# Optimization experiments

Hardware: AMD Instinct MI355X
Metric: run time of the kernel (lower is better)

## Reference

```python
import jax, jax.numpy as jnp
import numpy as np

EPS = 1e-8


def setup_inputs() -> dict:
    key = jax.random.key(0)
    ks = jax.random.split(key, 4)
    B, Cin, Cout, K, S, H, W = 16, 256, 256, 3, 512, 128, 128
    return {
        "x": jax.random.normal(ks[0], (B, Cin, H, W), dtype=jnp.float32),
        "style": jax.random.normal(ks[1], (B, S), dtype=jnp.float32),
        "weight": jax.random.normal(ks[2], (1, Cout, Cin, K, K), dtype=jnp.float32),
        "mod_w": jax.random.normal(ks[3], (Cin, S), dtype=jnp.float32) * (1.0 / np.sqrt(S)),
        "mod_b": jnp.zeros((Cin,), dtype=jnp.float32),
        "bias": jnp.zeros((1, Cout, 1, 1), dtype=jnp.float32),
    }


def reference(x, style, weight, mod_w, mod_b, bias):
    B, Cin, H, W = x.shape
    _, Cout, _, K, _ = weight.shape
    scale = 1.0 / np.sqrt(Cin * K * K)

    # modulation: Linear(style_dim -> in_channel)
    s = style @ mod_w.T + mod_b                      # [B, Cin]
    w = scale * weight * s[:, None, :, None, None]   # [B, Cout, Cin, K, K]
    demod = jax.lax.rsqrt(jnp.sum(w * w, axis=(2, 3, 4)) + EPS)  # [B, Cout]
    w = w * demod[:, :, None, None, None]

    # grouped conv with groups = batch (per-sample weights)
    w = w.reshape(B * Cout, Cin, K, K)
    xg = x.reshape(1, B * Cin, H, W)
    out = jax.lax.conv_general_dilated(
        xg, w,
        window_strides=(1, 1),
        padding=[(1, 1), (1, 1)],
        dimension_numbers=("NCHW", "OIHW", "NCHW"),
        feature_group_count=B,
    )
    Ho, Wo = out.shape[2], out.shape[3]
    out = out.reshape(B, Cout, Ho, Wo)
    return out + bias
```

## Files before the change

kernel.cpp:

```cpp
#include <hip/hip_runtime.h>
#include <stdint.h>

typedef unsigned short u16;
typedef __attribute__((ext_vector_type(8))) short short8;
typedef __attribute__((ext_vector_type(4))) float f32x4;

#define AS1 __attribute__((address_space(1)))
#define AS3 __attribute__((address_space(3)))

static __device__ __forceinline__ void gload_lds16(const void* g, void* l) {
  __builtin_amdgcn_global_load_lds((const AS1 void*)g, (AS3 void*)l, 16, 0, 0);
}

static __device__ __forceinline__ u16 bf16r(float f) {
  union { float f; uint32_t u; } c; c.f = f;
  uint32_t u = c.u;
  u += 0x7fffu + ((u >> 16) & 1u);
  return (u16)(u >> 16);
}

static constexpr int NB = 16, CIN = 256, COUT = 256, HW = 128, SDIM = 512;
static constexpr float SCALE = 1.0f / 48.0f;

__global__ void k_style(const float* __restrict__ style, const float* __restrict__ mod_w,
                        const float* __restrict__ mod_b, float* __restrict__ s) {
  int b = blockIdx.x, ci = threadIdx.x;
  const float4* st = (const float4*)(style + (size_t)b * SDIM);
  const float4* mw = (const float4*)(mod_w + (size_t)ci * SDIM);
  float acc = 0.f;
  #pragma unroll 4
  for (int j = 0; j < SDIM / 4; ++j) {
    float4 a = st[j], w = mw[j];
    acc += a.x * w.x + a.y * w.y + a.z * w.z + a.w * w.w;
  }
  s[b * CIN + ci] = acc + mod_b[ci];
}

__global__ void k_wmod(const float* __restrict__ weight, const float* __restrict__ s,
                       u16* __restrict__ Wb) {
  __shared__ float wld[CIN * 9];
  __shared__ float red[8];
  int bid = blockIdx.x;
  int b = bid >> 8, co = bid & 255;
  int t = threadIdx.x;
  const float* wsrc = weight + (size_t)co * (CIN * 9);
  for (int i = t; i < CIN * 9; i += 256) wld[i] = wsrc[i];
  __syncthreads();
  int ci = t;
  float sv = s[b * CIN + ci];
  float v[9];
  float sq = 0.f;
  #pragma unroll
  for (int k = 0; k < 9; ++k) {
    float w = SCALE * wld[ci * 9 + k] * sv;
    v[k] = w;
    sq += w * w;
  }
  #pragma unroll
  for (int off = 32; off; off >>= 1) sq += __shfl_down(sq, off);
  int lane = t & 63, wid = t >> 6;
  if (lane == 0) red[wid] = sq;
  __syncthreads();
  if (t == 0) red[4] = rsqrtf(red[0] + red[1] + red[2] + red[3] + 1e-8f);
  __syncthreads();
  float demod = red[4];
  #pragma unroll
  for (int k = 0; k < 9; ++k) {
    Wb[(((size_t)b * 9 + k) * COUT + co) * CIN + ci] = bf16r(v[k] * demod);
  }
}

__global__ void k_xt(const float* __restrict__ x, u16* __restrict__ xTp) {
  __shared__ u16 T[128 * 65];
  int bid = blockIdx.x;
  int b = bid >> 7, h = bid & 127;
  int t = threadIdx.x;
  size_t rowbase = ((size_t)b * 130 + (h + 1)) * 130 * CIN;
  xTp[rowbase + t] = 0;
  xTp[rowbase + (size_t)129 * CIN + t] = 0;
  if (h == 0) {
    uint32_t* g = (uint32_t*)(xTp + (size_t)b * 130 * 130 * CIN);
    for (int i = t; i < 130 * CIN / 2; i += 256) g[i] = 0;
  }
  if (h == 127) {
    uint32_t* g = (uint32_t*)(xTp + ((size_t)b * 130 + 129) * 130 * CIN);
    for (int i = t; i < 130 * CIN / 2; i += 256) g[i] = 0;
  }
  for (int ci0 = 0; ci0 < CIN; ci0 += 64) {
    __syncthreads();
    #pragma unroll
    for (int i = 0; i < 8; ++i) {
      int idx = t + i * 256;
      int ci = idx >> 5, px4 = idx & 31;
      float4 v = *(const float4*)(x + (((size_t)b * CIN + ci0 + ci) * HW + h) * HW + px4 * 4);
      T[(px4 * 4 + 0) * 65 + ci] = bf16r(v.x);
      T[(px4 * 4 + 1) * 65 + ci] = bf16r(v.y);
      T[(px4 * 4 + 2) * 65 + ci] = bf16r(v.z);
      T[(px4 * 4 + 3) * 65 + ci] = bf16r(v.w);
    }
    __syncthreads();
    int ci = t & 63, pxo = t >> 6;
    #pragma unroll
    for (int i = 0; i < 32; ++i) {
      int px = i * 4 + pxo;
      xTp[rowbase + (size_t)(px + 1) * CIN + ci0 + ci] = T[px * 65 + ci];
    }
  }
}

static constexpr int SLOT = 12288;

__global__ __launch_bounds__(256, 2) void k_conv(const u16* __restrict__ Wb,
                                                 const u16* __restrict__ xTp,
                                                 const float* __restrict__ bias,
                                                 float* __restrict__ out) {
  extern __shared__ u16 lds[];
  int bid = blockIdx.x;
  int swz = (bid & 7) * 256 + (bid >> 3);
  int b = swz >> 7, r = swz & 127;
  int c2 = r >> 6, hp = r & 63;
  int h0 = hp * 2, co0 = c2 * 128;

  int t = threadIdx.x, lane = t & 63, wid = t >> 6;
  int wc = wid;
  int l15 = lane & 15;
  int row0 = wid * 16 + (lane >> 2);
  int sq8 = ((lane & 3) ^ ((lane >> 3) & 3)) << 3;
  int aswz = (((lane >> 4) ^ ((l15 >> 1) & 3))) << 3;
  const u16* Ab = Wb + (size_t)b * 9 * 65536;
  const u16* Bx = xTp + (size_t)b * 130 * 130 * 256;

  f32x4 acc[8][4];
  #pragma unroll
  for (int i = 0; i < 8; ++i)
    #pragma unroll
    for (int j = 0; j < 4; ++j) acc[i][j] = (f32x4)0.f;

#define STAGE(KT, SN)                                                            \
  do {                                                                           \
    int kpos_ = (KT) >> 3, ci0_ = ((KT) & 7) << 5;                               \
    int kh_ = kpos_ < 3 ? 0 : (kpos_ < 6 ? 1 : 2);                               \
    int kw_ = kpos_ - kh_ * 3;                                                   \
    const u16* As_ = Ab + (size_t)kpos_ * 65536 +                                \
                     (size_t)(co0 + row0) * 256 + ci0_ + sq8;                    \
    gload_lds16(As_,         (SN) + wid * 512 + lane * 8);                       \
    gload_lds16(As_ + 16384, (SN) + 2048 + wid * 512 + lane * 8);                \
    _Pragma("unroll")                                                            \
    for (int i_ = 0; i_ < 4; ++i_) {                                             \
      int r_ = i_ * 64 + row0;                                                   \
      const u16* Bs_ = Bx + ((size_t)(h0 + kh_ + (r_ >> 7)) * 130 + kw_          \
                             + (r_ & 127)) * 256 + ci0_ + sq8;                   \
      gload_lds16(Bs_, (SN) + 4096 + i_ * 2048 + wid * 512 + lane * 8);          \
    }                                                                            \
  } while (0)

#define KTBODY(KT, SCUR, SNXT)                                                   \
  {                                                                              \
    if ((KT) + 1 < 72) STAGE((KT) + 1, SNXT);                                    \
    short8 af_[8], bf_[4];                                                       \
    _Pragma("unroll")                                                            \
    for (int mt = 0; mt < 8; ++mt)                                               \
      af_[mt] = *(const short8*)&(SCUR)[mt * 512 + l15 * 32 + aswz];             \
    _Pragma("unroll")                                                            \
    for (int nt = 0; nt < 4; ++nt)                                               \
      bf_[nt] = *(const short8*)&(SCUR)[4096 + wc * 2048 + nt * 512              \
                                        + l15 * 32 + aswz];                      \
    __builtin_amdgcn_s_setprio(1);                                               \
    _Pragma("unroll")                                                            \
    for (int mt = 0; mt < 8; ++mt)                                               \
      _Pragma("unroll")                                                          \
      for (int nt = 0; nt < 4; ++nt)                                             \
        acc[mt][nt] = __builtin_amdgcn_mfma_f32_16x16x32_bf16(af_[mt], bf_[nt],  \
                                                              acc[mt][nt], 0, 0, 0); \
    __builtin_amdgcn_s_setprio(0);                                               \
    __syncthreads();                                                             \
  }

  u16* S0 = lds;
  u16* S1 = lds + SLOT;
  STAGE(0, S0);
  __syncthreads();

  #pragma unroll 1
  for (int kt = 0; kt < 72; kt += 2) {
    KTBODY(kt, S0, S1);
    KTBODY(kt + 1, S1, S0);
  }
#undef STAGE
#undef KTBODY

  #pragma unroll
  for (int mt = 0; mt < 8; ++mt) {
    #pragma unroll
    for (int j = 0; j < 4; ++j) {
      int co = co0 + mt * 16 + ((lane >> 4) * 4) + j;
      float bv = bias[co];
      #pragma unroll
      for (int nt = 0; nt < 4; ++nt) {
        int px = wc * 64 + nt * 16 + l15;
        int h = h0 + (px >> 7), w = px & 127;
        out[(((size_t)b * COUT + co) * HW + h) * HW + w] = acc[mt][nt][j] + bv;
      }
    }
  }
}

extern "C" void kernel_launch(void* const* d_in, const int* in_sizes, int n_in,
                              void* d_out, int out_size, void* d_ws, size_t ws_size,
                              hipStream_t stream) {
  const float* x      = (const float*)d_in[0];
  const float* style  = (const float*)d_in[1];
  const float* weight = (const float*)d_in[2];
  const float* mod_w  = (const float*)d_in[3];
  const float* mod_b  = (const float*)d_in[4];
  const float* bias   = (const float*)d_in[5];
  float* out = (float*)d_out;

  char* ws = (char*)d_ws;
  float* s   = (float*)ws;
  u16* Wb    = (u16*)(ws + 16384);
  u16* xTp   = (u16*)(ws + 16384 + (size_t)NB * 9 * COUT * CIN * 2);

  k_style<<<NB, 256, 0, stream>>>(style, mod_w, mod_b, s);
  k_wmod<<<NB * COUT, 256, 0, stream>>>(weight, s, Wb);
  k_xt<<<NB * HW, 256, 0, stream>>>(x, xTp);
  k_conv<<<NB * 2 * (HW / 2), 256, 2 * SLOT * 2, stream>>>(Wb, xTp, bias, out);
}
```

Baseline: 495.8 us.

## Retile conv to 256 channels by one row per block and vectorize xT stores

The conv kernel's block tile changes from 128 output channels by two image rows to all 256 output channels by a single row of 128 pixels. Waves are arranged 2x2 over channels and pixels, and the A/B staging in LDS is rearranged to match. Each input row slice is now loaded once for all channels, cutting redundant activation traffic, while the A/B tile ratio and total load per block shift. Separately, the transpose kernel now writes 16-byte vectors instead of scalar u16 stores.

```diff
diff --git a/kernel.cpp b/kernel.cpp
--- a/kernel.cpp
+++ b/kernel.cpp
@@ -86,6 +86,7 @@
     uint32_t* g = (uint32_t*)(xTp + ((size_t)b * 130 + 129) * 130 * CIN);
     for (int i = t; i < 130 * CIN / 2; i += 256) g[i] = 0;
   }
+  int c8 = t & 7, pxb = t >> 3;
   for (int ci0 = 0; ci0 < CIN; ci0 += 64) {
     __syncthreads();
     #pragma unroll
@@ -99,11 +100,13 @@
       T[(px4 * 4 + 3) * 65 + ci] = bf16r(v.w);
     }
     __syncthreads();
-    int ci = t & 63, pxo = t >> 6;
-    #pragma unroll
-    for (int i = 0; i < 32; ++i) {
-      int px = i * 4 + pxo;
-      xTp[rowbase + (size_t)(px + 1) * CIN + ci0 + ci] = T[px * 65 + ci];
+    #pragma unroll
+    for (int i = 0; i < 4; ++i) {
+      int px = i * 32 + pxb;
+      short8 v;
+      #pragma unroll
+      for (int j = 0; j < 8; ++j) v[j] = (short)T[px * 65 + c8 * 8 + j];
+      *(short8*)&xTp[rowbase + (size_t)(px + 1) * CIN + ci0 + c8 * 8] = v;
     }
   }
 }
@@ -117,16 +120,13 @@
   extern __shared__ u16 lds[];
   int bid = blockIdx.x;
   int swz = (bid & 7) * 256 + (bid >> 3);
-  int b = swz >> 7, r = swz & 127;
-  int c2 = r >> 6, hp = r & 63;
-  int h0 = hp * 2, co0 = c2 * 128;
+  int b = swz >> 7, h0 = swz & 127;
 
   int t = threadIdx.x, lane = t & 63, wid = t >> 6;
-  int wc = wid;
-  int l15 = lane & 15;
-  int row0 = wid * 16 + (lane >> 2);
-  int sq8 = ((lane & 3) ^ ((lane >> 3) & 3)) << 3;
-  int aswz = (((lane >> 4) ^ ((l15 >> 1) & 3))) << 3;
+  int wr = wid >> 1, wc = wid & 1;
+  int l15 = lane & 15, seg = lane >> 4;
+  int xq = ((seg ^ ((l15 >> 1) & 3))) << 3;
+  int ssrc8 = ((lane & 3) ^ ((lane >> 3) & 3)) << 3;
   const u16* Ab = Wb + (size_t)b * 9 * 65536;
   const u16* Bx = xTp + (size_t)b * 130 * 130 * 256;
 
@@ -141,16 +141,18 @@
     int kpos_ = (KT) >> 3, ci0_ = ((KT) & 7) << 5;                               \
     int kh_ = kpos_ < 3 ? 0 : (kpos_ < 6 ? 1 : 2);                               \
     int kw_ = kpos_ - kh_ * 3;                                                   \
-    const u16* As_ = Ab + (size_t)kpos_ * 65536 +                                \
-                     (size_t)(co0 + row0) * 256 + ci0_ + sq8;                    \
-    gload_lds16(As_,         (SN) + wid * 512 + lane * 8);                       \
-    gload_lds16(As_ + 16384, (SN) + 2048 + wid * 512 + lane * 8);                \
+    const u16* As_ = Ab + (size_t)kpos_ * 65536 + ci0_ + ssrc8;                  \
     _Pragma("unroll")                                                            \
     for (int i_ = 0; i_ < 4; ++i_) {                                             \
-      int r_ = i_ * 64 + row0;                                                   \
-      const u16* Bs_ = Bx + ((size_t)(h0 + kh_ + (r_ >> 7)) * 130 + kw_          \
-                             + (r_ & 127)) * 256 + ci0_ + sq8;                   \
-      gload_lds16(Bs_, (SN) + 4096 + i_ * 2048 + wid * 512 + lane * 8);          \
+      int row_ = (wid * 4 + i_) * 16 + (lane >> 2);                              \
+      gload_lds16(As_ + (size_t)row_ * 256, (SN) + (wid * 4 + i_) * 512 + lane * 8); \
+    }                                                                            \
+    const u16* Bs_ = Bx + ((size_t)(h0 + kh_) * 130 + kw_) * 256 + ci0_ + ssrc8; \
+    _Pragma("unroll")                                                            \
+    for (int i_ = 0; i_ < 2; ++i_) {                                             \
+      int r_ = (wid * 2 + i_) * 16 + (lane >> 2);                                \
+      gload_lds16(Bs_ + (size_t)r_ * 256,                                        \
+                  (SN) + 8192 + (wid * 2 + i_) * 512 + lane * 8);                \
     }                                                                            \
   } while (0)
 
@@ -160,11 +162,11 @@
     short8 af_[8], bf_[4];                                                       \
     _Pragma("unroll")                                                            \
     for (int mt = 0; mt < 8; ++mt)                                               \
-      af_[mt] = *(const short8*)&(SCUR)[mt * 512 + l15 * 32 + aswz];             \
+      af_[mt] = *(const short8*)&(SCUR)[(wr * 8 + mt) * 512 + l15 * 32 + xq];    \
     _Pragma("unroll")                                                            \
     for (int nt = 0; nt < 4; ++nt)                                               \
-      bf_[nt] = *(const short8*)&(SCUR)[4096 + wc * 2048 + nt * 512              \
-                                        + l15 * 32 + aswz];                      \
+      bf_[nt] = *(const short8*)&(SCUR)[8192 + (wc * 4 + nt) * 512               \
+                                        + l15 * 32 + xq];                        \
     __builtin_amdgcn_s_setprio(1);                                               \
     _Pragma("unroll")                                                            \
     for (int mt = 0; mt < 8; ++mt)                                               \
@@ -193,13 +195,12 @@
   for (int mt = 0; mt < 8; ++mt) {
     #pragma unroll
     for (int j = 0; j < 4; ++j) {
-      int co = co0 + mt * 16 + ((lane >> 4) * 4) + j;
+      int co = wr * 128 + mt * 16 + seg * 4 + j;
       float bv = bias[co];
       #pragma unroll
       for (int nt = 0; nt < 4; ++nt) {
         int px = wc * 64 + nt * 16 + l15;
-        int h = h0 + (px >> 7), w = px & 127;
-        out[(((size_t)b * COUT + co) * HW + h) * HW + w] = acc[mt][nt][j] + bv;
+        out[(((size_t)b * COUT + co) * HW + h0) * HW + px] = acc[mt][nt][j] + bv;
       }
     }
   }
@@ -221,8 +222,11 @@
   u16* Wb    = (u16*)(ws + 16384);
   u16* xTp   = (u16*)(ws + 16384 + (size_t)NB * 9 * COUT * CIN * 2);
 
+  (void)hipFuncSetAttribute((const void*)k_conv,
+                            hipFuncAttributeMaxDynamicSharedMemorySize, 2 * SLOT * 2);
+
   k_style<<<NB, 256, 0, stream>>>(style, mod_w, mod_b, s);
   k_wmod<<<NB * COUT, 256, 0, stream>>>(weight, s, Wb);
   k_xt<<<NB * HW, 256, 0, stream>>>(x, xTp);
-  k_conv<<<NB * 2 * (HW / 2), 256, 2 * SLOT * 2, stream>>>(Wb, xTp, bias, out);
-}
+  k_conv<<<NB * HW, 256, 2 * SLOT * 2, stream>>>(Wb, xTp, bias, out);
+}
```

Result: faster. 444.3 us (-10.4%).
